# Optimization experiments

Measured on AMD Instinct MI355X. Metric: run time of the kernel, lower is better.

The kernel has to match this reference:

```python
import jax, jax.numpy as jnp
import numpy as np

GRID_NUM = 5   # number of grid intervals (pykan default)
SPLINE_K = 3   # B-spline degree (pykan default)
GRID_RANGE = (-1.0, 1.0)


def make_grid(in_dim):
    # Extended uniform grid: num + 2k + 1 knots per input dim, shared values.
    h = (GRID_RANGE[1] - GRID_RANGE[0]) / GRID_NUM
    pts = GRID_RANGE[0] + h * jnp.arange(-SPLINE_K, GRID_NUM + SPLINE_K + 1, dtype=jnp.float32)
    return jnp.broadcast_to(pts, (in_dim, pts.shape[0]))  # (in_dim, num+2k+1)


def bspline_basis(x, grid, k):
    # Cox-de Boor recursion. x: (n, d); grid: (d, m). Returns (n, d, m-1-k).
    xe = x[..., None]            # (n, d, 1)
    g = grid[None]               # (1, d, m)
    B = ((xe >= g[..., :-1]) & (xe < g[..., 1:])).astype(x.dtype)
    for p in range(1, k + 1):
        left = (xe - g[..., :-(p + 1)]) / (g[..., p:-1] - g[..., :-(p + 1)])
        right = (g[..., p + 1:] - xe) / (g[..., p + 1:] - g[..., 1:-p])
        B = left * B[..., :-1] + right * B[..., 1:]
    return B


def kan_layer(x, coef, scale_base, scale_sp, grid):
    # x: (n, in); coef: (in, out, G+k); scales: (in, out)
    basis = bspline_basis(x, grid, SPLINE_K)              # (n, in, G+k)
    base = jax.nn.silu(x)                                 # (n, in)
    # y[n,o] = sum_i scale_base[i,o]*silu(x[n,i]) + scale_sp[i,o]*sum_g B[n,i,g]*coef[i,o,g]
    spline = jnp.einsum('nig,iog->no', basis, coef * scale_sp[:, :, None])
    return base @ scale_base + spline


def setup_inputs() -> dict:
    key = jax.random.key(0)
    ks = jax.random.split(key, 5)
    b, s, hid, ffn = 2, 4096, 512, 2048
    nb = GRID_NUM + SPLINE_K  # 8 basis functions
    x = jax.random.normal(ks[0], (b, s, hid), dtype=jnp.float32)
    coef1 = 0.1 * jax.random.normal(ks[1], (hid, ffn, nb), dtype=jnp.float32)
    scale_base1 = (1.0 / np.sqrt(hid)) * jax.random.normal(ks[2], (hid, ffn), dtype=jnp.float32)
    scale_sp1 = jnp.ones((hid, ffn), dtype=jnp.float32)
    coef2 = 0.1 * jax.random.normal(ks[3], (ffn, hid, nb), dtype=jnp.float32)
    scale_base2 = (1.0 / np.sqrt(ffn)) * jax.random.normal(ks[4], (ffn, hid), dtype=jnp.float32)
    scale_sp2 = jnp.ones((ffn, hid), dtype=jnp.float32)
    return {'x': x, 'coef1': coef1, 'scale_base1': scale_base1, 'scale_sp1': scale_sp1,
            'coef2': coef2, 'scale_base2': scale_base2, 'scale_sp2': scale_sp2}


def reference(x, coef1, scale_base1, scale_sp1, coef2, scale_base2, scale_sp2):
    b, s, hid = x.shape
    ffn = coef1.shape[1]
    grid1 = make_grid(hid)   # non-trainable buffers, derived from defaults
    grid2 = make_grid(ffn)
    h = x.reshape(b * s, hid)                     # rearrange 'b s h -> (b s) h'
    h = kan_layer(h, coef1, scale_base1, scale_sp1, grid1)
    h = kan_layer(h, coef2, scale_base2, scale_sp2, grid2)
    return h.reshape(b, s, hid)
```

## Files before the change

kernel.cpp:

```cpp
#include <hip/hip_runtime.h>
#include <cstdint>
#include <cstddef>

typedef _Float16 f16;
typedef _Float16 f16x8 __attribute__((ext_vector_type(8)));
typedef float f32x4 __attribute__((ext_vector_type(4)));


template <int I, int O>
__global__ void prep_coef(const float* __restrict__ coef,
                          const float* __restrict__ ssp,
                          f16* __restrict__ Wt) {
  constexpr int K32 = (9 * I) / 32;
  int tid = blockIdx.x * 256 + threadIdx.x;
  if (tid >= I * O) return;
  int i = tid / O, o = tid % O;
  float s = ssp[tid];
  const float* c = coef + (size_t)tid * 8;
  f16x8 out;
#pragma unroll
  for (int g = 0; g < 8; ++g) out[g] = (f16)(c[g] * s);
  size_t addr = ((size_t)(o >> 4) * K32 + (i >> 2)) * 512 +
                (size_t)(((i & 3) * 16) + (o & 15)) * 8;
  *(f16x8*)(Wt + addr) = out;
}

template <int I, int O>
__global__ void prep_base(const float* __restrict__ sb, f16* __restrict__ Wt) {
  constexpr int K32 = (9 * I) / 32;
  int tid = blockIdx.x * 256 + threadIdx.x;
  if (tid >= (I / 8) * O) return;
  int i8 = tid / O, o = tid % O;
  f16x8 out;
#pragma unroll
  for (int s = 0; s < 8; ++s)
    out[s] = (f16)sb[(size_t)(i8 * 8 + s) * O + o];
  size_t addr = ((size_t)(o >> 4) * K32 + (I / 4) + (i8 >> 2)) * 512 +
                (size_t)(((i8 & 3) * 16) + (o & 15)) * 8;
  *(f16x8*)(Wt + addr) = out;
}

__device__ __forceinline__ f16x8 spline8(float h) {
  float v = __builtin_fmaf(2.5f, h, 5.5f);
  float c = floorf(v);
  float f = v - c;
  float f2 = f * f, f3 = f2 * f;
  float b3 = f3 * (1.f / 6.f);
  float t = 1.f - f;
  float b0 = t * t * t * (1.f / 6.f);
  float b1 = (2.f / 3.f) - f2 + 0.5f * f3;
  float b2 = 1.f - b0 - b1 - b3;
  unsigned int u01 =
      __builtin_bit_cast(unsigned int, __builtin_amdgcn_cvt_pkrtz(b0, b1));
  unsigned int u23 =
      __builtin_bit_cast(unsigned int, __builtin_amdgcn_cvt_pkrtz(b2, b3));
  unsigned long long pk = (unsigned long long)u01 |
                          ((unsigned long long)u23 << 32);
  int ci = (int)c;
  int s = (ci - 3) * 16;
  __uint128_t r = 0;
  if (s >= 0) {
    if (s < 128) r = (__uint128_t)pk << s;
  } else {
    int q = -s;
    if (q < 64) r = (__uint128_t)(pk >> q);
  }
  return __builtin_bit_cast(f16x8, r);
}

template <int I, int ATOMIC>
__global__ __launch_bounds__(256, 2) void gemm_kan(const float* __restrict__ H,
                                                   const f16* __restrict__ W,
                                                   float* __restrict__ C,
                                                   int N, int kChunk) {
  constexpr int K = 9 * I;
  constexpr int KB = 8 * I;
  constexpr int K32 = K / 32;
  __shared__ __align__(16) f16 sA[128 * 64];
  const int t = threadIdx.x;
  const int n0 = blockIdx.x * 256;
  const int m0 = blockIdx.y * 128;
  const int kBeg = blockIdx.z * kChunk;
  const int kEnd = kBeg + kChunk;
  const int w = t >> 6, lane = t & 63;
  const int wm = (w >> 1) * 64, wn = (w & 1) * 128;
  const int lr = lane & 15, lq = lane >> 4;
  const int srow = t >> 3;
  const int j_ = t & 7;
  const int js = j_ ^ (srow & 7);

  f32x4 acc[4][8] = {};
  const float* Hrow = H + (size_t)(m0 + srow) * I;
  const f16* Pw = W + (size_t)((n0 + wn) >> 4) * K32 * 512 + lane * 8;

  float hs[4];
  if (kBeg < KB) {
    const int i0 = kBeg >> 3;
#pragma unroll
    for (int q = 0; q < 4; ++q)
      hs[q] = Hrow[(size_t)(q * 32) * I + i0 + j_];
  }

  for (int k0 = kBeg; k0 < kEnd; k0 += 64) {
    const int kb0 = k0 >> 5;
    f16x8 bv0[8];
#pragma unroll
    for (int j = 0; j < 8; ++j)
      bv0[j] = *(const f16x8*)(Pw + ((size_t)j * K32 + kb0) * 512);

    if (k0 < KB) {
#pragma unroll
      for (int q = 0; q < 4; ++q)
        *(f16x8*)&sA[((q * 32 + srow) * 8 + js) * 8] = spline8(hs[q]);
      const int kn = k0 + 64;
      if (kn < kEnd && kn < KB) {
        const int i0n = kn >> 3;
#pragma unroll
        for (int q = 0; q < 4; ++q)
          hs[q] = Hrow[(size_t)(q * 32) * I + i0n + j_];
      }
    } else {
      const int c0 = (k0 - KB) + j_ * 8;
      f32x4 ha[4][2];
#pragma unroll
      for (int q = 0; q < 4; ++q) {
        const f32x4* p = (const f32x4*)(Hrow + (size_t)(q * 32) * I + c0);
        ha[q][0] = p[0];
        ha[q][1] = p[1];
      }
#pragma unroll
      for (int q = 0; q < 4; ++q) {
        f16x8 o;
#pragma unroll
        for (int s = 0; s < 8; ++s) {
          float h = ha[q][s >> 2][s & 3];
          o[s] = (f16)(h / (1.f + __expf(-h)));
        }
        *(f16x8*)&sA[((q * 32 + srow) * 8 + js) * 8] = o;
      }
    }
    __syncthreads();

    f16x8 av[4], bv1[8];
#pragma unroll
    for (int i = 0; i < 4; ++i) {
      const int ra = wm + i * 16 + lr;
      const int ca = lq ^ (ra & 7);
      av[i] = *(const f16x8*)&sA[ra * 64 + ca * 8];
    }
#pragma unroll
    for (int j = 0; j < 8; ++j)
      bv1[j] = *(const f16x8*)(Pw + ((size_t)j * K32 + kb0 + 1) * 512);
#pragma unroll
    for (int i = 0; i < 4; ++i)
#pragma unroll
      for (int j = 0; j < 8; ++j)
        acc[i][j] = __builtin_amdgcn_mfma_f32_16x16x32_f16(av[i], bv0[j],
                                                           acc[i][j], 0, 0, 0);
#pragma unroll
    for (int i = 0; i < 4; ++i) {
      const int ra = wm + i * 16 + lr;
      const int ca = (4 + lq) ^ (ra & 7);
      av[i] = *(const f16x8*)&sA[ra * 64 + ca * 8];
    }
#pragma unroll
    for (int i = 0; i < 4; ++i)
#pragma unroll
      for (int j = 0; j < 8; ++j)
        acc[i][j] = __builtin_amdgcn_mfma_f32_16x16x32_f16(av[i], bv1[j],
                                                           acc[i][j], 0, 0, 0);
    __syncthreads();
  }

#pragma unroll
  for (int i = 0; i < 4; ++i) {
#pragma unroll
    for (int j = 0; j < 8; ++j) {
      const int col = n0 + wn + j * 16 + lr;
#pragma unroll
      for (int r = 0; r < 4; ++r) {
        const int row = m0 + wm + i * 16 + lq * 4 + r;
        if (ATOMIC)
          atomicAdd(&C[(size_t)row * N + col], acc[i][j][r]);
        else
          C[(size_t)row * N + col] = acc[i][j][r];
      }
    }
  }
}

extern "C" void kernel_launch(void* const* d_in, const int* in_sizes, int n_in,
                              void* d_out, int out_size, void* d_ws,
                              size_t ws_size, hipStream_t stream) {
  const float* x     = (const float*)d_in[0];
  const float* coef1 = (const float*)d_in[1];
  const float* sb1   = (const float*)d_in[2];
  const float* ssp1  = (const float*)d_in[3];
  const float* coef2 = (const float*)d_in[4];
  const float* sb2   = (const float*)d_in[5];
  const float* ssp2  = (const float*)d_in[6];

  const int Mtot = 8192;
  const int I1 = 512, O1 = 2048, K1 = I1 * 9;
  const int I2 = 2048, O2 = 512, K2 = I2 * 9;

  char* ws = (char*)d_ws;
  const size_t szW1 = (size_t)O1 * K1 * sizeof(f16);
  const size_t szW2 = (size_t)O2 * K2 * sizeof(f16);
  const size_t szH  = (size_t)Mtot * O1 * sizeof(float);
  if (ws_size < szW1 + szW2 + szH) return;
  f16*   W1 = (f16*)ws;
  f16*   W2 = (f16*)(ws + szW1);
  float* h1 = (float*)(ws + szW1 + szW2);

  {
    int n1 = I1 * O1;
    prep_coef<512, 2048><<<(n1 + 255) / 256, 256, 0, stream>>>(coef1, ssp1, W1);
    prep_base<512, 2048><<<(n1 / 8 + 255) / 256, 256, 0, stream>>>(sb1, W1);
    int n2 = I2 * O2;
    prep_coef<2048, 512><<<(n2 + 255) / 256, 256, 0, stream>>>(coef2, ssp2, W2);
    prep_base<2048, 512><<<(n2 / 8 + 255) / 256, 256, 0, stream>>>(sb2, W2);
  }

  gemm_kan<512, 0><<<dim3(O1 / 256, Mtot / 128, 1), 256, 0, stream>>>(
      x, W1, h1, O1, K1);

  (void)hipMemsetAsync(d_out, 0, (size_t)Mtot * O2 * sizeof(float), stream);
  const int SK = 4;
  gemm_kan<2048, 1><<<dim3(O2 / 256, Mtot / 128, SK), 256, 0, stream>>>(
      h1, W2, (float*)d_out, O2, K2 / SK);
}
```

Measured before the change: 522.1 us.

## Double-buffer the A tile in shared memory to overlap basis generation with MFMA

Shared memory for the A operand becomes two buffers. The next k-step's spline or SiLU values are computed between the MFMA phases and written to the alternate buffer, which cuts each loop iteration to a single barrier. The goal is to hide the ALU work and global loads behind matrix-core execution. The cost is twice the LDS footprint (32KB per block) and extra live registers for bv1 and nx, which may push register pressure past the two-blocks-per-CU launch bound.

```diff
diff --git a/kernel.cpp b/kernel.cpp
--- a/kernel.cpp
+++ b/kernel.cpp
@@ -76,7 +76,7 @@
   constexpr int K = 9 * I;
   constexpr int KB = 8 * I;
   constexpr int K32 = K / 32;
-  __shared__ __align__(16) f16 sA[128 * 64];
+  __shared__ __align__(16) f16 sA[2][128 * 64];
   const int t = threadIdx.x;
   const int n0 = blockIdx.x * 256;
   const int m0 = blockIdx.y * 128;
@@ -92,76 +92,101 @@
   f32x4 acc[4][8] = {};
   const float* Hrow = H + (size_t)(m0 + srow) * I;
   const f16* Pw = W + (size_t)((n0 + wn) >> 4) * K32 * 512 + lane * 8;
-
-  float hs[4];
-  if (kBeg < KB) {
-    const int i0 = kBeg >> 3;
+  const f16* Pwk = Pw + (size_t)(kBeg >> 5) * 512;
+
+  {
+    f16x8 nx[4];
+    if (kBeg < KB) {
+      const int i0 = kBeg >> 3;
+#pragma unroll
+      for (int q = 0; q < 4; ++q) {
+        float h = Hrow[(size_t)(q * 32) * I + i0 + j_];
+        nx[q] = spline8(h);
+      }
+    } else {
+      const int c0 = (kBeg - KB) + j_ * 8;
+#pragma unroll
+      for (int q = 0; q < 4; ++q) {
+        const f32x4* pp = (const f32x4*)(Hrow + (size_t)(q * 32) * I + c0);
+        f32x4 a0 = pp[0], a1 = pp[1];
+        f16x8 o;
+#pragma unroll
+        for (int s = 0; s < 8; ++s) {
+          float h = (s < 4) ? a0[s & 3] : a1[s & 3];
+          o[s] = (f16)(h / (1.f + __expf(-h)));
+        }
+        nx[q] = o;
+      }
+    }
 #pragma unroll
     for (int q = 0; q < 4; ++q)
-      hs[q] = Hrow[(size_t)(q * 32) * I + i0 + j_];
-  }
-
-  for (int k0 = kBeg; k0 < kEnd; k0 += 64) {
-    const int kb0 = k0 >> 5;
-    f16x8 bv0[8];
-#pragma unroll
-    for (int j = 0; j < 8; ++j)
-      bv0[j] = *(const f16x8*)(Pw + ((size_t)j * K32 + kb0) * 512);
-
-    if (k0 < KB) {
-#pragma unroll
-      for (int q = 0; q < 4; ++q)
-        *(f16x8*)&sA[((q * 32 + srow) * 8 + js) * 8] = spline8(hs[q]);
-      const int kn = k0 + 64;
-      if (kn < kEnd && kn < KB) {
+      *(f16x8*)&sA[0][((q * 32 + srow) * 8 + js) * 8] = nx[q];
+  }
+  __syncthreads();
+
+  int p = 0;
+  for (int k0 = kBeg; k0 < kEnd; k0 += 64, p ^= 1) {
+    const f16* curA = &sA[p][0];
+    f16x8 bv0[8], bv1[8];
+#pragma unroll
+    for (int j = 0; j < 8; ++j) {
+      bv0[j] = *(const f16x8*)(Pwk + (size_t)j * (K32 * 512));
+      bv1[j] = *(const f16x8*)(Pwk + (size_t)j * (K32 * 512) + 512);
+    }
+
+    const int kn = k0 + 64;
+    const bool more = kn < kEnd;
+    float hs[4];
+    f16x8 nx[4];
+    bool nspline = false;
+    if (more) {
+      if (kn < KB) {
+        nspline = true;
         const int i0n = kn >> 3;
 #pragma unroll
         for (int q = 0; q < 4; ++q)
           hs[q] = Hrow[(size_t)(q * 32) * I + i0n + j_];
-      }
-    } else {
-      const int c0 = (k0 - KB) + j_ * 8;
-      f32x4 ha[4][2];
-#pragma unroll
-      for (int q = 0; q < 4; ++q) {
-        const f32x4* p = (const f32x4*)(Hrow + (size_t)(q * 32) * I + c0);
-        ha[q][0] = p[0];
-        ha[q][1] = p[1];
-      }
-#pragma unroll
-      for (int q = 0; q < 4; ++q) {
-        f16x8 o;
-#pragma unroll
-        for (int s = 0; s < 8; ++s) {
-          float h = ha[q][s >> 2][s & 3];
-          o[s] = (f16)(h / (1.f + __expf(-h)));
+      } else {
+        const int c0 = (kn - KB) + j_ * 8;
+#pragma unroll
+        for (int q = 0; q < 4; ++q) {
+          const f32x4* pp = (const f32x4*)(Hrow + (size_t)(q * 32) * I + c0);
+          f32x4 a0 = pp[0], a1 = pp[1];
+          f16x8 o;
+#pragma unroll
+          for (int s = 0; s < 8; ++s) {
+            float h = (s < 4) ? a0[s & 3] : a1[s & 3];
+            o[s] = (f16)(h / (1.f + __expf(-h)));
+          }
+          nx[q] = o;
         }
-        *(f16x8*)&sA[((q * 32 + srow) * 8 + js) * 8] = o;
-      }
-    }
-    __syncthreads();
-
-    f16x8 av[4], bv1[8];
+      }
+    }
+
+    f16x8 av[4];
 #pragma unroll
     for (int i = 0; i < 4; ++i) {
       const int ra = wm + i * 16 + lr;
       const int ca = lq ^ (ra & 7);
-      av[i] = *(const f16x8*)&sA[ra * 64 + ca * 8];
-    }
-#pragma unroll
-    for (int j = 0; j < 8; ++j)
-      bv1[j] = *(const f16x8*)(Pw + ((size_t)j * K32 + kb0 + 1) * 512);
+      av[i] = *(const f16x8*)&curA[ra * 64 + ca * 8];
+    }
 #pragma unroll
     for (int i = 0; i < 4; ++i)
 #pragma unroll
       for (int j = 0; j < 8; ++j)
         acc[i][j] = __builtin_amdgcn_mfma_f32_16x16x32_f16(av[i], bv0[j],
                                                            acc[i][j], 0, 0, 0);
+
+    if (nspline) {
+#pragma unroll
+      for (int q = 0; q < 4; ++q) nx[q] = spline8(hs[q]);
+    }
+
 #pragma unroll
     for (int i = 0; i < 4; ++i) {
       const int ra = wm + i * 16 + lr;
       const int ca = (4 + lq) ^ (ra & 7);
-      av[i] = *(const f16x8*)&sA[ra * 64 + ca * 8];
+      av[i] = *(const f16x8*)&curA[ra * 64 + ca * 8];
     }
 #pragma unroll
     for (int i = 0; i < 4; ++i)
@@ -169,6 +194,14 @@
       for (int j = 0; j < 8; ++j)
         acc[i][j] = __builtin_amdgcn_mfma_f32_16x16x32_f16(av[i], bv1[j],
                                                            acc[i][j], 0, 0, 0);
+
+    if (more) {
+      f16* altA = &sA[p ^ 1][0];
+#pragma unroll
+      for (int q = 0; q < 4; ++q)
+        *(f16x8*)&altA[((q * 32 + srow) * 8 + js) * 8] = nx[q];
+    }
+    Pwk += 1024;
     __syncthreads();
   }
 
```

Result: slower. 547.1 us (+4.8%).
